# Kernel tuning notes

Hardware: AMD Instinct MI355X
Metric: run time of the kernel (lower is better)

Reference implementation:

```python
import jax, jax.numpy as jnp
import numpy as np

K = 9          # kernel_size
CENTER = K // 2
EXTEND = 1.0   # extend_scope
B, C_IN, C_OUT, H, W = 2, 64, 64, 256, 256


def group_norm(x, w, b, groups, eps=1e-5):
    Bx, C, Hx, Wx = x.shape
    xg = x.reshape(Bx, groups, C // groups, Hx, Wx)
    m = xg.mean(axis=(2, 3, 4), keepdims=True)
    v = xg.var(axis=(2, 3, 4), keepdims=True)
    xn = ((xg - m) * jax.lax.rsqrt(v + eps)).reshape(Bx, C, Hx, Wx)
    return xn * w[None, :, None, None] + b[None, :, None, None]


def conv2d(x, w, b, stride, padding):
    y = jax.lax.conv_general_dilated(x, w, stride, padding,
                                     dimension_numbers=('NCHW', 'OIHW', 'NCHW'))
    return y + b[None, :, None, None]


def bilinear_sample(feat, iy, ix):
    # feat [B,C,H,W]; iy/ix pixel coords [B,Hg,Wg]; align_corners=True bilinear
    Hf, Wf = feat.shape[2], feat.shape[3]
    y0 = jnp.floor(iy); x0 = jnp.floor(ix)
    wy1 = iy - y0; wx1 = ix - x0
    wy0 = 1.0 - wy1; wx0 = 1.0 - wx1
    y0i = jnp.clip(y0, 0, Hf - 1).astype(jnp.int32)
    y1i = jnp.clip(y0 + 1, 0, Hf - 1).astype(jnp.int32)
    x0i = jnp.clip(x0, 0, Wf - 1).astype(jnp.int32)
    x1i = jnp.clip(x0 + 1, 0, Wf - 1).astype(jnp.int32)
    g = jax.vmap(lambda f, yi, xi: f[:, yi, xi])  # per-batch gather -> [B,C,Hg,Wg]
    return (g(feat, y0i, x0i) * (wy0 * wx0)[:, None]
            + g(feat, y0i, x1i) * (wy0 * wx1)[:, None]
            + g(feat, y1i, x0i) * (wy1 * wx0)[:, None]
            + g(feat, y1i, x1i) * (wy1 * wx1)[:, None])


def outward_cumsum(off):
    # off [B,K,H,W]: center row -> 0, cumulative sums outward from center
    lower = jnp.flip(jnp.cumsum(jnp.flip(off[:, :CENTER], axis=1), axis=1), axis=1)
    upper = jnp.cumsum(off[:, CENTER + 1:], axis=1)
    zero = jnp.zeros_like(off[:, :1])
    return jnp.concatenate([lower, zero, upper], axis=1)


def reference(x, w_off, b_off, gno_w, gno_b, w_dsc, b_dsc, gn_w, gn_b):
    Bx, _, Hx, Wx = x.shape
    # offset branch: conv3x3 -> GroupNorm(K, 2K) -> tanh
    offset = conv2d(x, w_off, b_off, (1, 1), ((1, 1), (1, 1)))
    offset = jnp.tanh(group_norm(offset, gno_w, gno_b, groups=K))
    y_off = offset[:, :K]                      # morph=0 uses the y half
    y_cum = outward_cumsum(y_off)              # [B,K,H,W]
    y_center = jnp.arange(Hx, dtype=x.dtype)[None, None, :, None]
    x_base = (jnp.arange(Wx, dtype=x.dtype)[None, None, None, :]
              + jnp.linspace(-CENTER, CENTER, K, dtype=x.dtype)[None, :, None, None])
    y_new = y_center + EXTEND * y_cum          # [B,K,H,W]
    x_new = jnp.broadcast_to(x_base, y_new.shape)
    # permute(0,2,1,3).reshape -> [B, K*H, W]
    ycoord = y_new.transpose(0, 2, 1, 3).reshape(Bx, Hx * K, Wx)
    xcoord = x_new.transpose(0, 2, 1, 3).reshape(Bx, Hx * K, Wx)
    # clamp to [0,max] then [-1,1] normalize + align_corners unnormalize == clamp
    iy = jnp.clip(ycoord, 0.0, Hx - 1.0)
    ix = jnp.clip(xcoord, 0.0, Wx - 1.0)
    deformed = bilinear_sample(x, iy, ix)      # [B,C,K*H,W]
    out = conv2d(deformed, w_dsc, b_dsc, (K, 1), 'VALID')  # [B,Cout,H,W]
    out = group_norm(out, gn_w, gn_b, groups=C_OUT // 4)
    return jax.nn.relu(out)


def setup_inputs() -> dict:
    key = jax.random.key(0)
    ks = jax.random.split(key, 3)
    return {
        'x': jax.random.normal(ks[0], (B, C_IN, H, W), dtype=jnp.float32),
        'w_off': jax.random.normal(ks[1], (2 * K, C_IN, 3, 3), dtype=jnp.float32) * 0.05,
        'b_off': jnp.zeros((2 * K,), dtype=jnp.float32),
        'gno_w': jnp.ones((2 * K,), dtype=jnp.float32),
        'gno_b': jnp.zeros((2 * K,), dtype=jnp.float32),
        'w_dsc': jax.random.normal(ks[2], (C_OUT, C_IN, K, 1), dtype=jnp.float32) * 0.05,
        'b_dsc': jnp.zeros((C_OUT,), dtype=jnp.float32),
        'gn_w': jnp.ones((C_OUT,), dtype=jnp.float32),
        'gn_b': jnp.zeros((C_OUT,), dtype=jnp.float32),
    }
```

## Files before the change

### kernel.cpp

```cpp
#include <hip/hip_runtime.h>
#include <hip/hip_fp16.h>
#include <math.h>

#define BB 2
#define CC 64
#define HH 256
#define WW 256
#define KK 9
#define NOFF 10
#define HW (HH*WW)

typedef __attribute__((ext_vector_type(8))) short s16x8;
typedef __attribute__((ext_vector_type(4))) float f32x4;

__device__ __forceinline__ unsigned lerp2h(unsigned a, unsigned b, __half2 fy2) {
    __half2 ah = *(__half2*)&a, bh = *(__half2*)&b;
    __half2 d = __hfma2(fy2, __hsub2(bh, ah), ah);
    return *(unsigned*)&d;
}

__device__ __forceinline__ float fast_tanh(float z) {
    float e = __builtin_amdgcn_exp2f(z * 2.885390081777927f);
    return 1.f - 2.f * __builtin_amdgcn_rcpf(e + 1.f);
}

__device__ __forceinline__ void swizzle_bhw(int g, int& b, int& h, int& wt) {
    int W = ((g & 7) << 8) | (g >> 3);
    b  = W >> 10;
    int rem = W & 1023;
    h  = rem >> 2;
    wt = rem & 3;
}



__global__ __launch_bounds__(256) void transpose_x_kernel(const float* __restrict__ x,
                                                          unsigned short* __restrict__ xTh,
                                                          const float* __restrict__ w_off,
                                                          const float* __restrict__ w_dsc,
                                                          unsigned short* __restrict__ woffB,
                                                          unsigned short* __restrict__ wdscB,
                                                          float* __restrict__ sums_off,
                                                          float* __restrict__ sums_out) {
    if (blockIdx.x >= 2048) {
        int idx = (blockIdx.x - 2048) * 256 + threadIdx.x;
        if (blockIdx.x == 2048) {
            int t = threadIdx.x;
            for (int i = t; i < 128 * 32; i += 256) sums_off[i] = 0.f;
            for (int i = t; i < 128 * 32; i += 256) sums_out[i] = 0.f;
        }
        if (idx < 18 * 64 * 8) {
            int kb = idx >> 9;
            int L  = (idx >> 3) & 63;
            int j  = idx & 7;
            int n = L & 15, quad = L >> 4;
            int kk = kb * 32 + quad * 8 + j;
            int tap = kk >> 6, ci = kk & 63;
            float v = (n < NOFF) ? w_off[(n * 64 + ci) * 9 + tap] : 0.f;
            __half hv = __float2half(v);
            woffB[idx] = *(unsigned short*)&hv;
        }
        if (idx < 4 * 18 * 64 * 8) {
            int nt = idx / 9216;
            int r  = idx - nt * 9216;
            int kb = r >> 9;
            int L  = (r >> 3) & 63;
            int j  = r & 7;
            int n = L & 15, quad = L >> 4;
            int co = nt * 16 + n;
            int kk = kb * 32 + quad * 8 + j;
            int k = kk >> 6, ci = kk & 63;
            __half hv = __float2half(w_dsc[(co * 64 + ci) * 9 + k]);
            wdscB[idx] = *(unsigned short*)&hv;
        }
        return;
    }
    __shared__ float tile[64 * 65];
    int wt = blockIdx.x & 3;
    int h  = (blockIdx.x >> 2) & 255;
    int b  = blockIdx.x >> 10;
    int w0 = wt * 64;
    int t  = threadIdx.x;
    {
        int wq = t & 15, c0 = t >> 4;
#pragma unroll
        for (int it = 0; it < 4; ++it) {
            int c = c0 + it * 16;
            float4 v = *(const float4*)&x[(((b * CC + c) * HH + h) * WW) + w0 + wq * 4];
            tile[(wq * 4 + 0) * 65 + c] = v.x;
            tile[(wq * 4 + 1) * 65 + c] = v.y;
            tile[(wq * 4 + 2) * 65 + c] = v.z;
            tile[(wq * 4 + 3) * 65 + c] = v.w;
        }
    }
    __syncthreads();
    {
        int c8 = t & 7, wr = t >> 3;
        uint4* dst = (uint4*)xTh;
#pragma unroll
        for (int it = 0; it < 2; ++it) {
            int wl = wr + it * 32;
            const float* row = &tile[wl * 65 + c8 * 8];
            __half2 p0 = __floats2half2_rn(row[0], row[1]);
            __half2 p1 = __floats2half2_rn(row[2], row[3]);
            __half2 p2 = __floats2half2_rn(row[4], row[5]);
            __half2 p3 = __floats2half2_rn(row[6], row[7]);
            uint4 d;
            d.x = *(unsigned*)&p0; d.y = *(unsigned*)&p1;
            d.z = *(unsigned*)&p2; d.w = *(unsigned*)&p3;
            dst[((size_t)((b * HH + h) * WW) + w0 + wl) * 8 + c8] = d;
        }
    }
}

#define CPITCH 72
__global__ __launch_bounds__(256) void conv_off_mfma(const unsigned short* __restrict__ xTh,
                                                     const unsigned short* __restrict__ woffB,
                                                     const float* __restrict__ b_off,
                                                     unsigned short* __restrict__ off_raw,
                                                     float* __restrict__ sums_off) {
    __shared__ unsigned short sx[3 * 66 * CPITCH];
    __shared__ float rs[4][16], rs2[4][16];
    int t = threadIdx.x;
    int L = t & 63, v = t >> 6;
    int b, h, wt;
    swizzle_bhw(blockIdx.x, b, h, wt);
    int w0 = wt << 6;
    int col = L & 15, quad = L >> 4;

#pragma unroll
    for (int it = 0; it < 7; ++it) {
        int linear = it * 256 + t;
        if (linear < 1584) {
            int dy  = linear / 528;
            int rem = linear - dy * 528;
            int px  = rem >> 3, cg = rem & 7;
            int y  = h - 1 + dy;
            int xc = w0 - 1 + px;
            uint4 d = make_uint4(0, 0, 0, 0);
            if ((unsigned)y < 256u && (unsigned)xc < 256u)
                d = *(const uint4*)(xTh + ((size_t)(((b << 8) + y) << 8) + xc) * 64 + cg * 8);
            *(uint4*)&sx[(dy * 66 + px) * CPITCH + cg * 8] = d;
        }
    }

    s16x8 breg[18];
#pragma unroll
    for (int kb = 0; kb < 18; ++kb)
        breg[kb] = *(const s16x8*)(woffB + (kb * 64 + L) * 8);
    __syncthreads();

    f32x4 acc = {0.f, 0.f, 0.f, 0.f};
    __builtin_amdgcn_s_setprio(1);
#pragma unroll
    for (int kb = 0; kb < 18; ++kb) {
        int tap = kb >> 1;
        int dy = tap / 3, dxl = tap % 3;
        int pxl = v * 16 + col + dxl;
        int ci0 = ((kb & 1) << 5) + quad * 8;
        s16x8 a = *(const s16x8*)&sx[(dy * 66 + pxl) * CPITCH + ci0];
        acc = __builtin_amdgcn_mfma_f32_16x16x32_f16(a, breg[kb], acc, 0, 0, 0);
    }
    __builtin_amdgcn_s_setprio(0);
    int oc = col;
    float bo = b_off[oc];
    float s = 0.f, s2 = 0.f;
#pragma unroll
    for (int r = 0; r < 4; ++r) {
        float val = acc[r] + bo;
        if (oc < NOFF) {
            int w = w0 + v * 16 + quad * 4 + r;
            __half hv = __float2half(val);
            off_raw[((b * NOFF + oc) << 16) + (h << 8) + w] = *(unsigned short*)&hv;
        }
        s += val; s2 += val * val;
    }
    s  += __shfl_xor(s, 16, 64);  s  += __shfl_xor(s, 32, 64);
    s2 += __shfl_xor(s2, 16, 64); s2 += __shfl_xor(s2, 32, 64);
    if (quad == 0) { rs[v][oc] = s; rs2[v][oc] = s2; }
    __syncthreads();
    if (t < NOFF) {
        float a_ = rs[0][t] + rs[1][t] + rs[2][t] + rs[3][t];
        float a2 = rs2[0][t] + rs2[1][t] + rs2[2][t] + rs2[3][t];
        float* dst = sums_off + ((b << 6) + (blockIdx.x & 63)) * 32 + (t >> 1) * 2;
        atomicAdd(&dst[0], a_);
        atomicAdd(&dst[1], a2);
    }
}

__global__ __launch_bounds__(256) void main_mfma(const unsigned short* __restrict__ xTh,
                                                 const unsigned short* __restrict__ off_raw,
                                                 const float* __restrict__ sums_off,
                                                 const float* __restrict__ gno_w,
                                                 const float* __restrict__ gno_b,
                                                 const unsigned short* __restrict__ wdscB,
                                                 const float* __restrict__ b_dsc,
                                                 unsigned short* __restrict__ tmph,
                                                 float* __restrict__ sums_out) {
    __shared__ unsigned short aT[16 * 584];
    __shared__ uint2 coordP[576];

    int t = threadIdx.x;
    int L = t & 63, nt = t >> 6;
    int b, h, wt;
    swizzle_bhw(blockIdx.x, b, h, wt);
    int w0 = wt << 6;
    int bBase = b << 22;

    if (t < 64) {
        float sv[10];
        const float* p = sums_off + ((b << 6) + t) * 32;
#pragma unroll
        for (int i = 0; i < 10; ++i) sv[i] = p[i];
#pragma unroll
        for (int o = 1; o <= 32; o <<= 1) {
#pragma unroll
            for (int i = 0; i < 10; ++i) sv[i] += __shfl_xor(sv[i], o, 64);
        }
        float msg[5], rsg[5];
#pragma unroll
        for (int g = 0; g < 5; ++g) {
            float mean = sv[g * 2] * (1.f / 131072.f);
            float var  = sv[g * 2 + 1] * (1.f / 131072.f) - mean * mean;
            msg[g] = mean;
            rsg[g] = rsqrtf(var + 1e-5f);
        }
        int w = w0 + t;
        float tk[9];
#pragma unroll
        for (int k = 0; k < 9; ++k) {
            unsigned short u = off_raw[((b * NOFF + k) << 16) + (h << 8) + w];
            float vv = __half2float(*(__half*)&u);
            int g = k >> 1;
            tk[k] = fast_tanh((vv - msg[g]) * rsg[g] * gno_w[k] + gno_b[k]);
        }
        float yc[9];
        float c = 0.f;
#pragma unroll
        for (int k = 3; k >= 0; --k) { c += tk[k]; yc[k] = c; }
        yc[4] = 0.f;
        c = 0.f;
#pragma unroll
        for (int k = 5; k < 9; ++k) { c += tk[k]; yc[k] = c; }
#pragma unroll
        for (int k = 0; k < 9; ++k) {
            float y = fminf(fmaxf((float)h + yc[k], 0.f), 255.f);
            float y0f = floorf(y);
            int y0 = (int)y0f;
            int xc = min(max(w + k - 4, 0), 255);
            __half fh = __float2half(y - y0f);
            coordP[t * 9 + k] = make_uint2((unsigned)(bBase + (y0 << 14) + (xc << 6)),
                                           (unsigned)(*(unsigned short*)&fh));
        }
    }

    s16x8 wreg[18];
#pragma unroll
    for (int kb = 0; kb < 18; ++kb)
        wreg[kb] = *(const s16x8*)(wdscB + ((nt * 18 + kb) * 64 + L) * 8);

    int col = L & 15, quad = L >> 4;
    int co = nt * 16 + col;
    float bias = b_dsc[co];
    float ss = 0.f, ss2 = 0.f;

    int tt = t >> 3, cg = t & 7;
    int r2a[5], wadr[5];
#pragma unroll
    for (int it = 0; it < 5; ++it) {
        int r2 = it * 32 + tt;
        r2a[it] = r2;
        int pxl = r2 / 9, k = r2 - pxl * 9;
        wadr[it] = pxl * 584 + k * 64 + (((cg + k) & 7) << 3);
    }

    uint2 rc[5];
    uint4 u0[5], u1[5];

    auto issue = [&](int rr) {
#pragma unroll
        for (int it = 0; it < 5; ++it) {
            if (it < 4 || t < 128) {
                uint2 c2v = coordP[rr * 144 + r2a[it]];
                rc[it] = c2v;
                unsigned o0 = c2v.x + (cg << 3);
                unsigned o1 = c2v.y ? o0 + 16384 : o0;
                u0[it] = *(const uint4*)(xTh + o0);
                u1[it] = *(const uint4*)(xTh + o1);
            }
        }
    };
    auto consume = [&]() {
#pragma unroll
        for (int it = 0; it < 5; ++it) {
            if (it < 4 || t < 128) {
                unsigned short fb = (unsigned short)rc[it].y;
                __half fh = *(__half*)&fb;
                __half2 fy2 = __half2half2(fh);
                uint4 d;
                d.x = lerp2h(u0[it].x, u1[it].x, fy2);
                d.y = lerp2h(u0[it].y, u1[it].y, fy2);
                d.z = lerp2h(u0[it].z, u1[it].z, fy2);
                d.w = lerp2h(u0[it].w, u1[it].w, fy2);
                *(uint4*)&aT[wadr[it]] = d;
            }
        }
    };

    __syncthreads();
    issue(0);

    for (int r = 0; r < 4; ++r) {
        consume();
        __syncthreads();
        if (r < 3) issue(r + 1);

        {
            int row = col;
            f32x4 acc = {0.f, 0.f, 0.f, 0.f};
            __builtin_amdgcn_s_setprio(1);
#pragma unroll
            for (int kb = 0; kb < 18; ++kb) {
                int k  = kb >> 1;
                int cch = ((kb & 1) << 2) + quad;
                int c2 = (cch + k) & 7;
                s16x8 a = *(const s16x8*)&aT[row * 584 + k * 64 + c2 * 8];
                acc = __builtin_amdgcn_mfma_f32_16x16x32_f16(a, wreg[kb], acc, 0, 0, 0);
            }
            __builtin_amdgcn_s_setprio(0);
            int wblk = (w0 >> 2) + r * 4 + quad;
            size_t ebase = ((size_t)(((b << 8) + h) << 6) + wblk) * 64 + co;
            float v0 = acc[0] + bias, v1 = acc[1] + bias;
            float v2 = acc[2] + bias, v3 = acc[3] + bias;
            ss  += v0 + v1 + v2 + v3;
            ss2 += v0 * v0 + v1 * v1 + v2 * v2 + v3 * v3;
            __half2 p0 = __floats2half2_rn(v0, v1);
            __half2 p1 = __floats2half2_rn(v2, v3);
            uint2 pk;
            pk.x = *(unsigned*)&p0;
            pk.y = *(unsigned*)&p1;
            ((uint2*)tmph)[ebase] = pk;
        }
        if (r < 3) __syncthreads();
    }
    ss  += __shfl_xor(ss, 16, 64);  ss  += __shfl_xor(ss, 32, 64);
    ss2 += __shfl_xor(ss2, 16, 64); ss2 += __shfl_xor(ss2, 32, 64);
    float sg = ss, sg2 = ss2;
    sg  += __shfl_xor(sg, 1, 64);  sg  += __shfl_xor(sg, 2, 64);
    sg2 += __shfl_xor(sg2, 1, 64); sg2 += __shfl_xor(sg2, 2, 64);
    if (quad == 0 && (col & 3) == 0) {
        int gi = nt * 4 + (col >> 2);
        float* dst = sums_out + ((b << 6) + (blockIdx.x & 63)) * 32 + gi * 2;
        atomicAdd(&dst[0], sg);
        atomicAdd(&dst[1], sg2);
    }
}

__global__ __launch_bounds__(256) void apply_final_kernel(const unsigned short* __restrict__ tmph,
                                                          const float* __restrict__ sums_out,
                                                          const float* __restrict__ gn_w,
                                                          const float* __restrict__ gn_b,
                                                          float* __restrict__ out) {
    __shared__ float tile[64 * 65];
    __shared__ float statsS[32];
    int wt = blockIdx.x & 3;
    int h  = (blockIdx.x >> 2) & 255;
    int b  = blockIdx.x >> 10;
    int w0 = wt * 64;
    int t  = threadIdx.x;
    {
        int i8 = t >> 3, sb = t & 7;
        float s = 0.f;
#pragma unroll
        for (int bk = sb; bk < 64; bk += 8)
            s += sums_out[((b << 6) + bk) * 32 + i8];
        s += __shfl_xor(s, 1, 64); s += __shfl_xor(s, 2, 64); s += __shfl_xor(s, 4, 64);
        if (sb == 0) statsS[i8] = s;
    }
    __syncthreads();
    {
        int co = t & 63, wb0 = t >> 6;
        int g = co >> 2;
        float s0 = statsS[g * 2], s1 = statsS[g * 2 + 1];
        float mean = s0 * (1.f / 262144.f);
        float var  = s1 * (1.f / 262144.f) - mean * mean;
        float rstd = rsqrtf(var + 1e-5f);
        float sc = rstd * gn_w[co];
        float sh = gn_b[co] - mean * sc;
        const uint2* src = (const uint2*)tmph;
#pragma unroll
        for (int it = 0; it < 4; ++it) {
            int wb = wb0 + it * 4;
            size_t bp = (size_t)(((b << 8) + h) << 6) + (w0 >> 2) + wb;
            uint2 u = src[bp * 64 + co];
            float2 f0 = __half22float2(*(__half2*)&u.x);
            float2 f1 = __half22float2(*(__half2*)&u.y);
            float* dst = &tile[co * 65 + wb * 4];
            dst[0] = fmaxf(fmaf(f0.x, sc, sh), 0.f);
            dst[1] = fmaxf(fmaf(f0.y, sc, sh), 0.f);
            dst[2] = fmaxf(fmaf(f1.x, sc, sh), 0.f);
            dst[3] = fmaxf(fmaf(f1.y, sc, sh), 0.f);
        }
    }
    __syncthreads();
    {
        int wq = t & 15, c0 = t >> 4;
#pragma unroll
        for (int it = 0; it < 4; ++it) {
            int co = c0 + it * 16;
            const float* row = &tile[co * 65 + wq * 4];
            float4 v;
            v.x = row[0]; v.y = row[1]; v.z = row[2]; v.w = row[3];
            *(float4*)&out[((size_t)(b * CC + co) * HH + h) * WW + w0 + wq * 4] = v;
        }
    }
}

extern "C" void kernel_launch(void* const* d_in, const int* in_sizes, int n_in,
                              void* d_out, int out_size, void* d_ws, size_t ws_size,
                              hipStream_t stream) {
    const float* x     = (const float*)d_in[0];
    const float* w_off = (const float*)d_in[1];
    const float* b_off = (const float*)d_in[2];
    const float* gno_w = (const float*)d_in[3];
    const float* gno_b = (const float*)d_in[4];
    const float* w_dsc = (const float*)d_in[5];
    const float* b_dsc = (const float*)d_in[6];
    const float* gn_w  = (const float*)d_in[7];
    const float* gn_b  = (const float*)d_in[8];
    float* out = (float*)d_out;

    char* ws = (char*)d_ws;
    unsigned short* xTh     = (unsigned short*)(ws);
    unsigned short* tmph    = (unsigned short*)(ws + 16777216);
    unsigned short* off_raw = (unsigned short*)(ws + 33554432);
    unsigned short* wdscB   = (unsigned short*)(ws + 36175872);
    unsigned short* woffB   = (unsigned short*)(ws + 36249600);
    float* sums_off         = (float*)(ws + 36268032);
    float* sums_out         = (float*)(ws + 36284416);

    hipLaunchKernelGGL(transpose_x_kernel, dim3(2192), dim3(256), 0, stream,
                       x, xTh, w_off, w_dsc, woffB, wdscB, sums_off, sums_out);
    hipLaunchKernelGGL(conv_off_mfma, dim3(2048), dim3(256), 0, stream,
                       xTh, woffB, b_off, off_raw, sums_off);
    hipLaunchKernelGGL(main_mfma, dim3(2048), dim3(256), 0, stream,
                       xTh, off_raw, sums_off, gno_w, gno_b, wdscB, b_dsc,
                       tmph, sums_out);
    hipLaunchKernelGGL(apply_final_kernel, dim3(2048), dim3(256), 0, stream,
                       tmph, sums_out, gn_w, gn_b, out);
}
```

Measured before the change: 147.2 us.

## Double-buffer LDS tile and prefetch two rounds of gathers ahead in main_mfma

The single shared A-tile becomes two ping-pong buffers, and global gathers are issued two rounds ahead into two register sets. The MFMA on one buffer now runs while the other buffer is being filled, and one barrier per round is removed. The aim is to hide gather latency and barrier stalls. In exchange it doubles LDS use for the tile and roughly doubles the prefetch registers, which can reduce occupancy.

```diff
diff --git a/kernel.cpp b/kernel.cpp
--- a/kernel.cpp
+++ b/kernel.cpp
@@ -197,7 +197,7 @@
                                                  const float* __restrict__ b_dsc,
                                                  unsigned short* __restrict__ tmph,
                                                  float* __restrict__ sums_out) {
-    __shared__ unsigned short aT[16 * 584];
+    __shared__ unsigned short aT[2][16 * 584];
     __shared__ uint2 coordP[576];
 
     int t = threadIdx.x;
@@ -274,10 +274,10 @@
         wadr[it] = pxl * 584 + k * 64 + (((cg + k) & 7) << 3);
     }
 
-    uint2 rc[5];
-    uint4 u0[5], u1[5];
-
-    auto issue = [&](int rr) {
+    uint2 rcA[5]; uint4 u0A[5], u1A[5];
+    uint2 rcB[5]; uint4 u0B[5], u1B[5];
+
+    auto issue = [&](int rr, uint2 (&rc)[5], uint4 (&u0)[5], uint4 (&u1)[5]) {
 #pragma unroll
         for (int it = 0; it < 5; ++it) {
             if (it < 4 || t < 128) {
@@ -290,7 +290,8 @@
             }
         }
     };
-    auto consume = [&]() {
+    auto consume = [&](uint2 (&rc)[5], uint4 (&u0)[5], uint4 (&u1)[5],
+                       unsigned short* buf) {
 #pragma unroll
         for (int it = 0; it < 5; ++it) {
             if (it < 4 || t < 128) {
@@ -302,20 +303,24 @@
                 d.y = lerp2h(u0[it].y, u1[it].y, fy2);
                 d.z = lerp2h(u0[it].z, u1[it].z, fy2);
                 d.w = lerp2h(u0[it].w, u1[it].w, fy2);
-                *(uint4*)&aT[wadr[it]] = d;
+                *(uint4*)&buf[wadr[it]] = d;
             }
         }
     };
 
     __syncthreads();
-    issue(0);
-
+    issue(0, rcA, u0A, u1A);
+    issue(1, rcB, u0B, u1B);
+    consume(rcA, u0A, u1A, &aT[0][0]);
+    __syncthreads();
+
+#pragma unroll
     for (int r = 0; r < 4; ++r) {
-        consume();
-        __syncthreads();
-        if (r < 3) issue(r + 1);
+        if (r == 0) issue(2, rcA, u0A, u1A);
+        if (r == 1) issue(3, rcB, u0B, u1B);
 
         {
+            const unsigned short* bufR = aT[r & 1];
             int row = col;
             f32x4 acc = {0.f, 0.f, 0.f, 0.f};
             __builtin_amdgcn_s_setprio(1);
@@ -324,7 +329,7 @@
                 int k  = kb >> 1;
                 int cch = ((kb & 1) << 2) + quad;
                 int c2 = (cch + k) & 7;
-                s16x8 a = *(const s16x8*)&aT[row * 584 + k * 64 + c2 * 8];
+                s16x8 a = *(const s16x8*)&bufR[row * 584 + k * 64 + c2 * 8];
                 acc = __builtin_amdgcn_mfma_f32_16x16x32_f16(a, wreg[kb], acc, 0, 0, 0);
             }
             __builtin_amdgcn_s_setprio(0);
@@ -341,7 +346,12 @@
             pk.y = *(unsigned*)&p1;
             ((uint2*)tmph)[ebase] = pk;
         }
-        if (r < 3) __syncthreads();
+
+        if (r < 3) {
+            if ((r & 1) == 0) consume(rcB, u0B, u1B, &aT[1][0]);
+            else              consume(rcA, u0A, u1A, &aT[0][0]);
+            __syncthreads();
+        }
     }
     ss  += __shfl_xor(ss, 16, 64);  ss  += __shfl_xor(ss, 32, 64);
     ss2 += __shfl_xor(ss2, 16, 64); ss2 += __shfl_xor(ss2, 32, 64);
```

Result: slower. 151.1 us (+2.6%).
